# Optimization experiments

Measured on AMD Instinct MI355X. Metric: run time of the kernel, lower is better.

The kernel has to match this reference:

```python
import jax, jax.numpy as jnp
import numpy as np

B, S, D_IN = 128, 196, 512
H, DK, RATIO = 8, 32, 4
DV = RATIO * DK                      # 128
QKV_DIM = H * (2 * DK + DV)          # 1536
PROJ_IN = H * DV                     # 1024
EPS = 1e-3                           # keras BatchNormalization default epsilon
SCALE = DK ** (-0.5)


def hard_swish(x):
    return x * jnp.clip(x + 3.0, 0.0, 6.0) * (1.0 / 6.0)


def setup_inputs() -> dict:
    key = jax.random.key(0)
    ks = jax.random.split(key, 12)
    inp = {
        "x": jax.random.normal(ks[0], (B, S, D_IN), dtype=jnp.float32),
        "W_qkv": jax.random.normal(ks[1], (D_IN, QKV_DIM), dtype=jnp.float32) * (D_IN ** -0.5),
        "b_qkv": jnp.zeros((QKV_DIM,), dtype=jnp.float32),
        "gamma1": jnp.ones((QKV_DIM,), dtype=jnp.float32),
        "beta1": jnp.zeros((QKV_DIM,), dtype=jnp.float32),
        "mean1": jax.random.normal(ks[2], (QKV_DIM,), dtype=jnp.float32) * 0.1,
        "var1": jax.random.uniform(ks[3], (QKV_DIM,), minval=0.5, maxval=1.5, dtype=jnp.float32),
        "W_proj": jax.random.normal(ks[4], (PROJ_IN, D_IN), dtype=jnp.float32) * (PROJ_IN ** -0.5),
        "b_proj": jnp.zeros((D_IN,), dtype=jnp.float32),
        "gamma2": jnp.ones((D_IN,), dtype=jnp.float32),
        "beta2": jnp.zeros((D_IN,), dtype=jnp.float32),
        "mean2": jax.random.normal(ks[5], (D_IN,), dtype=jnp.float32) * 0.1,
        "var2": jax.random.uniform(ks[6], (D_IN,), minval=0.5, maxval=1.5, dtype=jnp.float32),
    }
    return inp


def _bn(x, gamma, beta, mean, var):
    # inference-mode BatchNorm over the last (channel) axis
    return (x - mean) * jax.lax.rsqrt(var + EPS) * gamma + beta


def reference(x, W_qkv, b_qkv, gamma1, beta1, mean1, var1,
              W_proj, b_proj, gamma2, beta2, mean2, var2):
    # QKV projection + BN
    qkv = _bn(x @ W_qkv + b_qkv, gamma1, beta1, mean1, var1)      # [B,S,1536]
    qkv = qkv.reshape(B, S, H, 2 * DK + DV)
    q, k, v = jnp.split(qkv, [DK, 2 * DK], axis=3)                # [B,S,H,*]
    q = jnp.transpose(q, (0, 2, 1, 3))                            # [B,H,S,DK]
    k = jnp.transpose(k, (0, 2, 1, 3))
    v = jnp.transpose(v, (0, 2, 1, 3))                            # [B,H,S,DV]
    attn = jax.nn.softmax(jnp.einsum("bhqd,bhkd->bhqk", q, k) * SCALE, axis=-1)
    av = jnp.einsum("bhqk,bhkd->bhqd", attn, v)                   # [B,H,S,DV]
    # faithful to original: transpose to [B,H,DV,S] then reshape to [B,S,H*DV]
    hidden = jnp.transpose(av, (0, 1, 3, 2)).reshape(B, S, PROJ_IN)
    hidden = hard_swish(hidden)
    out = _bn(hidden @ W_proj + b_proj, gamma2, beta2, mean2, var2)  # [B,S,512]
    return out
```

## Files before the change

### kernel.cpp

```cpp
#include <hip/hip_runtime.h>
#include <math.h>

namespace {

constexpr int Bb   = 128;
constexpr int Ss   = 196;
constexpr int DIN  = 512;
constexpr int Hh   = 8;
constexpr int DKc  = 32;
constexpr int DVc  = 128;
constexpr int QKVD = 1536;
constexpr int PIN  = 1024;
constexpr int Mrows = Bb * Ss;
constexpr float EPSc   = 1e-3f;
constexpr float SCALEc = 0.17677669529663687f;

typedef __bf16 bf16x8 __attribute__((ext_vector_type(8)));
typedef __bf16 bf16x4 __attribute__((ext_vector_type(4)));
typedef float  f32x4  __attribute__((ext_vector_type(4)));

constexpr int VT_STRIDE = 232;
constexpr size_t VT_QELEMS = 8192;
constexpr size_t VT_BH = 4 * VT_QELEMS;

__device__ __forceinline__ void gl_lds16(const void* g, void* l) {
    __builtin_amdgcn_global_load_lds(
        (const __attribute__((address_space(1))) void*)g,
        (__attribute__((address_space(3))) void*)l, 16, 0, 0);
}

__global__ __launch_bounds__(256)
void cvt_f32_bf16(const float* __restrict__ in, __bf16* __restrict__ out, int n4)
{
    int i = blockIdx.x * 256 + threadIdx.x;
    if (i < n4) {
        float4 v = ((const float4*)in)[i];
        bf16x4 o = { (__bf16)v.x, (__bf16)v.y, (__bf16)v.z, (__bf16)v.w };
        ((bf16x4*)out)[i] = o;
    }
}

__global__ __launch_bounds__(256)
void transpose_cvt(const float* __restrict__ W, __bf16* __restrict__ WT, int K, int N)
{
    __shared__ float tile[32][33];
    const int n0 = blockIdx.x * 32, k0 = blockIdx.y * 32;
    const int tx = threadIdx.x & 31, ty = threadIdx.x >> 5;
#pragma unroll
    for (int i = ty; i < 32; i += 8)
        tile[i][tx] = W[(size_t)(k0 + i) * N + n0 + tx];
    __syncthreads();
#pragma unroll
    for (int i = ty; i < 32; i += 8)
        WT[(size_t)(n0 + i) * K + k0 + tx] = (__bf16)tile[tx][i];
}

__global__ __launch_bounds__(256)
void gemm1_bn_scatter(const __bf16* __restrict__ A, const __bf16* __restrict__ BT,
                      const float* __restrict__ bias, const float* __restrict__ gamma,
                      const float* __restrict__ beta, const float* __restrict__ mean,
                      const float* __restrict__ var,
                      __bf16* __restrict__ qkvO, __bf16* __restrict__ VTp)
{
    constexpr int N = QKVD, K = DIN;
    constexpr int BM = 128, BN = 128;
    __shared__ __align__(16) char sm[65536];

    const int t    = threadIdx.x;
    const int wave = t >> 6;
    const int lane = t & 63;
    const int lr   = lane & 15;
    const int q    = lane >> 4;

    constexpr int ntiles = N / BN;
    constexpr int nwg = 196 * ntiles;
    const int bid = (blockIdx.x & 7) * (nwg >> 3) + (blockIdx.x >> 3);
    const int m0 = (bid / ntiles) * BM;
    const int n0 = (bid % ntiles) * BN;
    const int wm = (wave & 1) * 64;
    const int wn = (wave >> 1) * 64;

    const __bf16* aG0 = A  + (size_t)(m0 + (t >> 2)) * K + (t & 3) * 8;
    const __bf16* aG1 = aG0 + (size_t)64 * K;
    const __bf16* bG0 = BT + (size_t)(n0 + (t >> 2)) * K + (t & 3) * 8;
    const __bf16* bG1 = bG0 + (size_t)64 * K;

    auto STAGE = [&](int k0, int cur) {
        char* lA = sm + cur * 16384 + wave * 1024;
        char* lB = sm + 32768 + cur * 16384 + wave * 1024;
        gl_lds16(aG0 + k0,      lA);
        gl_lds16(aG1 + k0,      lA + 4096);
        gl_lds16(aG0 + k0 + 32, lA + 8192);
        gl_lds16(aG1 + k0 + 32, lA + 8192 + 4096);
        gl_lds16(bG0 + k0,      lB);
        gl_lds16(bG1 + k0,      lB + 4096);
        gl_lds16(bG0 + k0 + 32, lB + 8192);
        gl_lds16(bG1 + k0 + 32, lB + 8192 + 4096);
    };

    f32x4 acc[4][4] = {};

    STAGE(0, 0);
    __syncthreads();
    int cur = 0;
    for (int k0 = 0; k0 < K; k0 += 64) {
        if (k0 + 64 < K) STAGE(k0 + 64, cur ^ 1);
        const __bf16* Abuf = (const __bf16*)(sm + cur * 16384);
        const __bf16* Bbuf = (const __bf16*)(sm + 32768 + cur * 16384);
#pragma unroll
        for (int kk = 0; kk < 2; ++kk) {
            bf16x8 aF[4], bF[4];
#pragma unroll
            for (int i = 0; i < 4; ++i)
                aF[i] = *(const bf16x8*)(Abuf + kk * 4096 + (wm + i * 16 + lr) * 32 + q * 8);
#pragma unroll
            for (int j = 0; j < 4; ++j)
                bF[j] = *(const bf16x8*)(Bbuf + kk * 4096 + (wn + j * 16 + lr) * 32 + q * 8);
#pragma unroll
            for (int i = 0; i < 4; ++i)
#pragma unroll
                for (int j = 0; j < 4; ++j)
                    acc[i][j] = __builtin_amdgcn_mfma_f32_16x16x32_bf16(
                        aF[i], bF[j], acc[i][j], 0, 0, 0);
        }
        __syncthreads();
        cur ^= 1;
    }

    const int tmod = n0 % 384;
    const int cq0  = (tmod == 0) ? 0 : (tmod == 128 ? 64 : -1);
    const int vc0  = (tmod == 0) ? 64 : 0;
    const int nv   = (tmod == 256) ? 128 : 64;
    const bool qk_wave = (tmod == 0) ? (wn == 0) : (tmod == 128 ? (wn == 64) : false);

    __bf16* qkreg = (__bf16*)sm;
    __bf16* vreg  = (__bf16*)(sm + ((nv == 128) ? 0 : 18432));
    const int vbase = (nv == 128) ? wn : 0;

#pragma unroll
    for (int j = 0; j < 4; ++j) {
        const int n = n0 + wn + j * 16 + lr;
        const float s  = gamma[n] * rsqrtf(var[n] + EPSc);
        const float tv = fmaf(bias[n] - mean[n], s, beta[n]);
        if (qk_wave) {
#pragma unroll
            for (int i = 0; i < 4; ++i) {
                const int row = wm + i * 16 + q * 4;
#pragma unroll
                for (int r = 0; r < 4; ++r)
                    qkreg[(row + r) * 72 + j * 16 + lr] = (__bf16)fmaf(acc[i][j][r], s, tv);
            }
        } else {
#pragma unroll
            for (int i = 0; i < 4; ++i) {
                bf16x4 pk = { (__bf16)fmaf(acc[i][j][0], s, tv),
                              (__bf16)fmaf(acc[i][j][1], s, tv),
                              (__bf16)fmaf(acc[i][j][2], s, tv),
                              (__bf16)fmaf(acc[i][j][3], s, tv) };
                *(bf16x4*)(vreg + (vbase + j * 16 + lr) * 136 + wm + i * 16 + q * 4) = pk;
            }
        }
    }
    __syncthreads();

    if (cq0 >= 0) {
#pragma unroll
        for (int rr = 0; rr < 4; ++rr) {
            const int row = rr * 32 + (t >> 3);
            const int l   = t & 7;
            bf16x8 vv = *(const bf16x8*)(qkreg + row * 72 + l * 8);
            *(bf16x8*)(qkvO + (size_t)(m0 + row) * N + n0 + cq0 + l * 8) = vv;
        }
    }
    const int iters = (nv * 16) / 256;
    for (int it = 0; it < iters; ++it) {
        const int a  = it * 256 + t;
        const int cl = a >> 4;
        const int r0 = (a & 15) * 8;
        const int n  = n0 + vc0 + cl;
        const int h  = n / 192;
        const int d  = n - h * 192 - 64;
        const int mr = m0 + r0;
        const int b_ = mr / 196;
        const int s0 = mr - b_ * 196;
        __bf16* dst0 = VTp + (size_t)(b_ * 8 + h) * VT_BH
                     + (size_t)(d >> 5) * VT_QELEMS + (size_t)(d & 31) * VT_STRIDE;
        bf16x8 vv = *(const bf16x8*)(vreg + cl * 136 + r0);
        if (s0 <= 188) {
            *(bf16x8*)(dst0 + s0) = vv;
        } else {
#pragma unroll
            for (int e = 0; e < 8; ++e) {
                int se = s0 + e;
                __bf16* dst = dst0;
                if (se >= 196) { se -= 196; dst += 8 * VT_BH; }
                dst[se] = vv[e];
            }
        }
    }
}

template<int N, int K>
__global__ __launch_bounds__(256)
void gemm_bn_mfma(const __bf16* __restrict__ A, const __bf16* __restrict__ BT,
                  const float* __restrict__ bias, const float* __restrict__ gamma,
                  const float* __restrict__ beta, const float* __restrict__ mean,
                  const float* __restrict__ var, float* __restrict__ C)
{
    constexpr int BM = 128, BN = 128;
    __shared__ __align__(16) char sm[65536];
    const int t    = threadIdx.x;
    const int wave = t >> 6;
    const int lane = t & 63;
    const int lr   = lane & 15;
    const int q    = lane >> 4;
    constexpr int ntiles = N / BN;
    constexpr int nwg = 196 * ntiles;
    const int bid = (blockIdx.x & 7) * (nwg >> 3) + (blockIdx.x >> 3);
    const int m0 = (bid / ntiles) * BM;
    const int n0 = (bid % ntiles) * BN;
    const int wm = (wave & 1) * 64;
    const int wn = (wave >> 1) * 64;
    const __bf16* aG0 = A  + (size_t)(m0 + (t >> 2)) * K + (t & 3) * 8;
    const __bf16* aG1 = aG0 + (size_t)64 * K;
    const __bf16* bG0 = BT + (size_t)(n0 + (t >> 2)) * K + (t & 3) * 8;
    const __bf16* bG1 = bG0 + (size_t)64 * K;

    auto STAGE = [&](int k0, int cur) {
        char* lA = sm + cur * 16384 + wave * 1024;
        char* lB = sm + 32768 + cur * 16384 + wave * 1024;
        gl_lds16(aG0 + k0,      lA);
        gl_lds16(aG1 + k0,      lA + 4096);
        gl_lds16(aG0 + k0 + 32, lA + 8192);
        gl_lds16(aG1 + k0 + 32, lA + 8192 + 4096);
        gl_lds16(bG0 + k0,      lB);
        gl_lds16(bG1 + k0,      lB + 4096);
        gl_lds16(bG0 + k0 + 32, lB + 8192);
        gl_lds16(bG1 + k0 + 32, lB + 8192 + 4096);
    };

    f32x4 acc[4][4] = {};

    STAGE(0, 0);
    __syncthreads();
    int cur = 0;
    for (int k0 = 0; k0 < K; k0 += 64) {
        if (k0 + 64 < K) STAGE(k0 + 64, cur ^ 1);
        const __bf16* Abuf = (const __bf16*)(sm + cur * 16384);
        const __bf16* Bbuf = (const __bf16*)(sm + 32768 + cur * 16384);
#pragma unroll
        for (int kk = 0; kk < 2; ++kk) {
            bf16x8 aF[4], bF[4];
#pragma unroll
            for (int i = 0; i < 4; ++i)
                aF[i] = *(const bf16x8*)(Abuf + kk * 4096 + (wm + i * 16 + lr) * 32 + q * 8);
#pragma unroll
            for (int j = 0; j < 4; ++j)
                bF[j] = *(const bf16x8*)(Bbuf + kk * 4096 + (wn + j * 16 + lr) * 32 + q * 8);
#pragma unroll
            for (int i = 0; i < 4; ++i)
#pragma unroll
                for (int j = 0; j < 4; ++j)
                    acc[i][j] = __builtin_amdgcn_mfma_f32_16x16x32_bf16(
                        aF[i], bF[j], acc[i][j], 0, 0, 0);
        }
        __syncthreads();
        cur ^= 1;
    }
#pragma unroll
    for (int j = 0; j < 4; ++j) {
        const int n = n0 + wn + j * 16 + lr;
        const float s  = gamma[n] * rsqrtf(var[n] + EPSc);
        const float tv = fmaf(bias[n] - mean[n], s, beta[n]);
#pragma unroll
        for (int i = 0; i < 4; ++i) {
            const int mrow = m0 + wm + i * 16 + q * 4;
#pragma unroll
            for (int r = 0; r < 4; ++r)
                C[(size_t)(mrow + r) * N + n] = fmaf(acc[i][j][r], s, tv);
        }
    }
}

__global__ __launch_bounds__(1024)
void attn_mfma(const __bf16* __restrict__ qkv, const __bf16* __restrict__ VTp,
               __bf16* __restrict__ hidden)
{
    __shared__ __align__(16) char smem[145920];
    __bf16* Kb = (__bf16*)smem;

    const int t = threadIdx.x;
    const int wave = t >> 6, lane = t & 63;
    const int lr = lane & 15, q = lane >> 4;
    const int bh = blockIdx.x;
    const int b = bh >> 3, h = bh & 7;
    const __bf16* qkvb = qkv + (size_t)b * 196 * QKVD + h * 192;

    const char* gV = (const char*)(VTp + (size_t)bh * VT_BH);
    char* ldsV = smem + 113152;
    gl_lds16(gV + wave * 1024 + lane * 16, ldsV + wave * 1024);

    if (t < 196 * 4) {
        const int s = t >> 2, c = t & 3;
        bf16x8 v = *(const bf16x8*)(qkvb + (size_t)s * QKVD + 32 + c * 8);
        *(bf16x8*)(Kb + s * 40 + c * 8) = v;
    }

    __syncthreads();

    const int qt = wave;
    const bool wactive = (qt <= 12);
    __bf16* Pw = (__bf16*)(smem + 16640 + (wactive ? qt : 0) * 7424);

    if (wactive) {
        int sQ = qt * 16 + lr; if (sQ > 195) sQ = 195;
        bf16x8 aQ = *(const bf16x8*)(qkv + ((size_t)b * 196 + sQ) * QKVD + h * 192 + q * 8);

        f32x4 sc[13];
#pragma unroll
        for (int nt = 0; nt < 13; ++nt) {
            bf16x8 bK = *(const bf16x8*)(Kb + (nt * 16 + lr) * 40 + q * 8);
            f32x4 z = {0.f, 0.f, 0.f, 0.f};
            sc[nt] = __builtin_amdgcn_mfma_f32_16x16x32_bf16(aQ, bK, z, 0, 0, 0);
        }
        float mrow[4] = {-1e30f, -1e30f, -1e30f, -1e30f};
#pragma unroll
        for (int nt = 0; nt < 13; ++nt) {
            const bool valid = (nt < 12) | (lr < 4);
#pragma unroll
            for (int r = 0; r < 4; ++r) {
                float x = sc[nt][r] * SCALEc;
                sc[nt][r] = x;
                if (valid) mrow[r] = fmaxf(mrow[r], x);
            }
        }
#pragma unroll
        for (int d = 1; d < 16; d <<= 1)
#pragma unroll
            for (int r = 0; r < 4; ++r)
                mrow[r] = fmaxf(mrow[r], __shfl_xor(mrow[r], d, 64));
        float l[4] = {0.f, 0.f, 0.f, 0.f};
#pragma unroll
        for (int nt = 0; nt < 13; ++nt) {
            const bool valid = (nt < 12) | (lr < 4);
#pragma unroll
            for (int r = 0; r < 4; ++r) {
                float e = valid ? __expf(sc[nt][r] - mrow[r]) : 0.f;
                sc[nt][r] = e;
                l[r] += e;
            }
        }
#pragma unroll
        for (int d = 1; d < 16; d <<= 1)
#pragma unroll
            for (int r = 0; r < 4; ++r)
                l[r] += __shfl_xor(l[r], d, 64);
        float inv[4];
#pragma unroll
        for (int r = 0; r < 4; ++r) inv[r] = 1.f / l[r];

#pragma unroll
        for (int nt = 0; nt < 13; ++nt)
#pragma unroll
            for (int r = 0; r < 4; ++r)
                Pw[(q * 4 + r) * 232 + nt * 16 + lr] = (__bf16)(sc[nt][r] * inv[r]);
        for (int idx = lane; idx < 16 * 24; idx += 64) {
            int row = idx & 15, cz = 208 + (idx >> 4);
            Pw[row * 232 + cz] = (__bf16)0.f;
        }
    }
    __syncthreads();

    const int sbase = qt * 16 + q * 4;
    const bool sval = wactive && (sbase + 3 < 196);
    __bf16* hb = hidden + (size_t)b * 200704 + (size_t)h * 25088;

    for (int q4 = 0; q4 < 4; ++q4) {
        const __bf16* Vl = (const __bf16*)(ldsV + (q4 & 1) * 16384);
        if (q4 < 3)
            gl_lds16(gV + (size_t)(q4 + 1) * 16384 + wave * 1024 + lane * 16,
                     ldsV + ((q4 + 1) & 1) * 16384 + wave * 1024);
        if (wactive) {
            f32x4 o0 = {0.f, 0.f, 0.f, 0.f}, o1 = {0.f, 0.f, 0.f, 0.f};
#pragma unroll
            for (int kk = 0; kk < 7; ++kk) {
                bf16x8 aP = *(const bf16x8*)(Pw + lr * 232 + kk * 32 + q * 8);
                bf16x8 b0 = *(const bf16x8*)(Vl + lr * 232 + kk * 32 + q * 8);
                bf16x8 b1 = *(const bf16x8*)(Vl + (16 + lr) * 232 + kk * 32 + q * 8);
                o0 = __builtin_amdgcn_mfma_f32_16x16x32_bf16(aP, b0, o0, 0, 0, 0);
                o1 = __builtin_amdgcn_mfma_f32_16x16x32_bf16(aP, b1, o1, 0, 0, 0);
            }
            if (sval) {
#pragma unroll
                for (int nt2 = 0; nt2 < 2; ++nt2) {
                    f32x4 o = nt2 ? o1 : o0;
                    const int d = q4 * 32 + nt2 * 16 + lr;
                    bf16x4 pk;
#pragma unroll
                    for (int r = 0; r < 4; ++r) {
                        float x = o[r];
                        pk[r] = (__bf16)(x * fminf(fmaxf(x + 3.f, 0.f), 6.f) * (1.f / 6.f));
                    }
                    *(bf16x4*)(hb + (size_t)d * 196 + sbase) = pk;
                }
            }
        }
        if (q4 < 3) __syncthreads();
    }
}

}

extern "C" void kernel_launch(void* const* d_in, const int* in_sizes, int n_in,
                              void* d_out, int out_size, void* d_ws, size_t ws_size,
                              hipStream_t stream)
{
    const float* x    = (const float*)d_in[0];
    const float* Wqkv = (const float*)d_in[1];
    const float* bqkv = (const float*)d_in[2];
    const float* g1   = (const float*)d_in[3];
    const float* be1  = (const float*)d_in[4];
    const float* mu1  = (const float*)d_in[5];
    const float* va1  = (const float*)d_in[6];
    const float* Wp   = (const float*)d_in[7];
    const float* bp   = (const float*)d_in[8];
    const float* g2   = (const float*)d_in[9];
    const float* be2  = (const float*)d_in[10];
    const float* mu2  = (const float*)d_in[11];
    const float* va2  = (const float*)d_in[12];

    char* ws = (char*)d_ws;
    __bf16* qkv    = (__bf16*)ws;
    __bf16* VTp    = (__bf16*)(ws + 77070336);
    __bf16* hidden = (__bf16*)(ws + 144179200);
    __bf16* xb     = (__bf16*)(ws + 195559424);
    __bf16* WT1    = (__bf16*)(ws + 221249536);
    __bf16* WT2    = (__bf16*)(ws + 222822400);
    float*  out    = (float*)d_out;

    cvt_f32_bf16<<<dim3((Mrows * DIN / 4 + 255) / 256), dim3(256), 0, stream>>>(
        x, xb, Mrows * DIN / 4);
    transpose_cvt<<<dim3(QKVD / 32, DIN / 32), dim3(256), 0, stream>>>(Wqkv, WT1, DIN, QKVD);
    transpose_cvt<<<dim3(DIN / 32, PIN / 32), dim3(256), 0, stream>>>(Wp, WT2, PIN, DIN);

    gemm1_bn_scatter<<<dim3(196 * (QKVD / 128)), dim3(256), 0, stream>>>(
        xb, WT1, bqkv, g1, be1, mu1, va1, qkv, VTp);

    attn_mfma<<<dim3(Bb * Hh), dim3(1024), 0, stream>>>(qkv, VTp, hidden);

    gemm_bn_mfma<DIN, PIN><<<dim3(196 * (DIN / 128)), dim3(256), 0, stream>>>(
        hidden, WT2, bp, g2, be2, mu2, va2, out);
}
```

Before: 281.8 us.

## Fuse fp32-to-bf16 conversion of x into GEMM1 loads and merge weight transposes

Removes the standalone conversion kernel for x. GEMM1 now loads fp32 activations into registers, converts them to bf16 and writes them to LDS during the double-buffered loop. The two weight transpose kernels are merged into a single launch. This saves a full read/write pass over x and two launches. In exchange, GEMM1 reads twice as many bytes for A per tile and uses more registers, since A no longer goes direct-to-LDS.

```diff
diff --git a/kernel.cpp b/kernel.cpp
--- a/kernel.cpp
+++ b/kernel.cpp
@@ -30,21 +30,15 @@
 }
 
 __global__ __launch_bounds__(256)
-void cvt_f32_bf16(const float* __restrict__ in, __bf16* __restrict__ out, int n4)
-{
-    int i = blockIdx.x * 256 + threadIdx.x;
-    if (i < n4) {
-        float4 v = ((const float4*)in)[i];
-        bf16x4 o = { (__bf16)v.x, (__bf16)v.y, (__bf16)v.z, (__bf16)v.w };
-        ((bf16x4*)out)[i] = o;
-    }
-}
-
-__global__ __launch_bounds__(256)
-void transpose_cvt(const float* __restrict__ W, __bf16* __restrict__ WT, int K, int N)
+void transpose_cvt2(const float* __restrict__ W1, __bf16* __restrict__ WT1o,
+                    const float* __restrict__ W2, __bf16* __restrict__ WT2o)
 {
     __shared__ float tile[32][33];
-    const int n0 = blockIdx.x * 32, k0 = blockIdx.y * 32;
+    int id = blockIdx.x;
+    const float* W; __bf16* WT; int K, N, bx, by;
+    if (id < 768) { W = W1; WT = WT1o; K = 512;  N = 1536; bx = id % 48; by = id / 48; }
+    else { id -= 768; W = W2; WT = WT2o; K = 1024; N = 512;  bx = id % 16; by = id / 16; }
+    const int n0 = bx * 32, k0 = by * 32;
     const int tx = threadIdx.x & 31, ty = threadIdx.x >> 5;
 #pragma unroll
     for (int i = ty; i < 32; i += 8)
@@ -56,7 +50,7 @@
 }
 
 __global__ __launch_bounds__(256)
-void gemm1_bn_scatter(const __bf16* __restrict__ A, const __bf16* __restrict__ BT,
+void gemm1_bn_scatter(const float* __restrict__ X, const __bf16* __restrict__ BT,
                       const float* __restrict__ bias, const float* __restrict__ gamma,
                       const float* __restrict__ beta, const float* __restrict__ mean,
                       const float* __restrict__ var,
@@ -80,18 +74,35 @@
     const int wm = (wave & 1) * 64;
     const int wn = (wave >> 1) * 64;
 
-    const __bf16* aG0 = A  + (size_t)(m0 + (t >> 2)) * K + (t & 3) * 8;
-    const __bf16* aG1 = aG0 + (size_t)64 * K;
+    const float*  xA  = X  + (size_t)(m0 + (t >> 2)) * K + (t & 3) * 8;
     const __bf16* bG0 = BT + (size_t)(n0 + (t >> 2)) * K + (t & 3) * 8;
     const __bf16* bG1 = bG0 + (size_t)64 * K;
 
-    auto STAGE = [&](int k0, int cur) {
-        char* lA = sm + cur * 16384 + wave * 1024;
+    float4 fa[4][2];
+    auto LOADA = [&](int k0) {
+        const float* p = xA + k0;
+        fa[0][0] = *(const float4*)(p);
+        fa[0][1] = *(const float4*)(p + 4);
+        fa[1][0] = *(const float4*)(p + 64 * K);
+        fa[1][1] = *(const float4*)(p + 64 * K + 4);
+        fa[2][0] = *(const float4*)(p + 32);
+        fa[2][1] = *(const float4*)(p + 36);
+        fa[3][0] = *(const float4*)(p + 64 * K + 32);
+        fa[3][1] = *(const float4*)(p + 64 * K + 36);
+    };
+    auto WRITEA = [&](int cur) {
+        char* base = sm + cur * 16384;
+#pragma unroll
+        for (int c = 0; c < 4; ++c) {
+            bf16x8 w = { (__bf16)fa[c][0].x, (__bf16)fa[c][0].y,
+                         (__bf16)fa[c][0].z, (__bf16)fa[c][0].w,
+                         (__bf16)fa[c][1].x, (__bf16)fa[c][1].y,
+                         (__bf16)fa[c][1].z, (__bf16)fa[c][1].w };
+            *(bf16x8*)(base + c * 4096 + t * 16) = w;
+        }
+    };
+    auto STAGEB = [&](int k0, int cur) {
         char* lB = sm + 32768 + cur * 16384 + wave * 1024;
-        gl_lds16(aG0 + k0,      lA);
-        gl_lds16(aG1 + k0,      lA + 4096);
-        gl_lds16(aG0 + k0 + 32, lA + 8192);
-        gl_lds16(aG1 + k0 + 32, lA + 8192 + 4096);
         gl_lds16(bG0 + k0,      lB);
         gl_lds16(bG1 + k0,      lB + 4096);
         gl_lds16(bG0 + k0 + 32, lB + 8192);
@@ -100,11 +111,12 @@
 
     f32x4 acc[4][4] = {};
 
-    STAGE(0, 0);
+    LOADA(0); STAGEB(0, 0); WRITEA(0);
     __syncthreads();
     int cur = 0;
     for (int k0 = 0; k0 < K; k0 += 64) {
-        if (k0 + 64 < K) STAGE(k0 + 64, cur ^ 1);
+        const bool next = (k0 + 64 < K);
+        if (next) { LOADA(k0 + 64); STAGEB(k0 + 64, cur ^ 1); }
         const __bf16* Abuf = (const __bf16*)(sm + cur * 16384);
         const __bf16* Bbuf = (const __bf16*)(sm + 32768 + cur * 16384);
 #pragma unroll
@@ -123,6 +135,7 @@
                     acc[i][j] = __builtin_amdgcn_mfma_f32_16x16x32_bf16(
                         aF[i], bF[j], acc[i][j], 0, 0, 0);
         }
+        if (next) WRITEA(cur ^ 1);
         __syncthreads();
         cur ^= 1;
     }
@@ -433,18 +446,14 @@
     __bf16* qkv    = (__bf16*)ws;
     __bf16* VTp    = (__bf16*)(ws + 77070336);
     __bf16* hidden = (__bf16*)(ws + 144179200);
-    __bf16* xb     = (__bf16*)(ws + 195559424);
     __bf16* WT1    = (__bf16*)(ws + 221249536);
     __bf16* WT2    = (__bf16*)(ws + 222822400);
     float*  out    = (float*)d_out;
 
-    cvt_f32_bf16<<<dim3((Mrows * DIN / 4 + 255) / 256), dim3(256), 0, stream>>>(
-        x, xb, Mrows * DIN / 4);
-    transpose_cvt<<<dim3(QKVD / 32, DIN / 32), dim3(256), 0, stream>>>(Wqkv, WT1, DIN, QKVD);
-    transpose_cvt<<<dim3(DIN / 32, PIN / 32), dim3(256), 0, stream>>>(Wp, WT2, PIN, DIN);
+    transpose_cvt2<<<dim3(1280), dim3(256), 0, stream>>>(Wqkv, WT1, Wp, WT2);
 
     gemm1_bn_scatter<<<dim3(196 * (QKVD / 128)), dim3(256), 0, stream>>>(
-        xb, WT1, bqkv, g1, be1, mu1, va1, qkv, VTp);
+        x, WT1, bqkv, g1, be1, mu1, va1, qkv, VTp);
 
     attn_mfma<<<dim3(Bb * Hh), dim3(1024), 0, stream>>>(qkv, VTp, hidden);
 
```

Result: slower. 301.7 us (+7.1%).
